# Kernel optimization log

Hardware: AMD Instinct MI355X
Metric: run time of the kernel (lower is better)

## Reference

```python
import jax, jax.numpy as jnp
import numpy as np
import math

FS = 9          # gaussian filter_size
STD = 1.0
LOW = 0.1       # min(threshold1, threshold2)
HIGH = 0.3      # max(threshold1, threshold2)
PAD_G = FS // 2


def _gauss_window(M, std):
    # scipy.signal.windows.gaussian: exp(-0.5*(n/std)^2), n centered, unnormalized
    n = np.arange(M, dtype=np.float64) - (M - 1) / 2.0
    return np.exp(-0.5 * (n / std) ** 2).astype(np.float32)


def _conv(x, w, pad):
    # torch F.conv2d == cross-correlation, NCHW / OIHW
    return jax.lax.conv_general_dilated(
        x, w, window_strides=(1, 1), padding=pad,
        dimension_numbers=("NCHW", "OIHW", "NCHW"))


def setup_inputs() -> dict:
    key = jax.random.key(0)
    img = jax.random.uniform(key, (8, 3, 512, 512), dtype=jnp.float32)
    g = _gauss_window(FS, STD)
    gauss_h = jnp.asarray(g[None, None, None, :])          # [1,1,1,9]
    gauss_v = jnp.asarray(g[None, None, :, None])          # [1,1,9,1]
    sobel_h = jnp.array([[[[1., 0., -1.], [2., 0., -2.], [1., 0., -1.]]]], dtype=jnp.float32)
    sobel_v = jnp.array([[[[1., 2., 1.], [0., 0., 0.], [-1., -2., -1.]]]], dtype=jnp.float32)
    d = np.zeros((8, 1, 3, 3), dtype=np.float32)
    d[:, 0, 1, 1] = 1.0
    # neighbor positions (row, col) for the -1 tap, per directional channel
    neigh = [(1, 2), (2, 2), (2, 1), (2, 0), (1, 0), (0, 0), (0, 1), (0, 2)]
    for k, (r, c) in enumerate(neigh):
        d[k, 0, r, c] = -1.0
    directional = jnp.asarray(d)                            # [8,1,3,3]
    connect = jnp.array([[[[1., 1., 1.], [1., 0., 1.], [1., 1., 1.]]]], dtype=jnp.float32)
    return {"img": img, "gauss_h": gauss_h, "gauss_v": gauss_v,
            "sobel_h": sobel_h, "sobel_v": sobel_v,
            "directional": directional, "connect": connect}


def reference(img, gauss_h, gauss_v, sobel_h, sobel_v, directional, connect):
    B, C, H, W = img.shape
    x = img.reshape(B * C, 1, H, W)  # per-channel 1-in/1-out convs, batched
    blur = _conv(_conv(x, gauss_h, [(0, 0), (PAD_G, PAD_G)]),
                 gauss_v, [(PAD_G, PAD_G), (0, 0)])
    gx = _conv(blur, sobel_h, [(1, 1), (1, 1)]).reshape(B, C, H, W)
    gy = _conv(blur, sobel_v, [(1, 1), (1, 1)]).reshape(B, C, H, W)

    # sum of per-channel magnitudes, [B,1,H,W]
    grad_mag = jnp.sqrt(gx * gx + gy * gy).sum(axis=1, keepdims=True)
    ori = jnp.arctan2(gy.sum(axis=1, keepdims=True),
                      gx.sum(axis=1, keepdims=True)) * (180.0 / math.pi) + 180.0
    ori = jnp.round(ori / 45.0) * 45.0

    all_filtered = _conv(grad_mag, directional, [(1, 1), (1, 1)])  # [B,8,H,W]

    pixel_count = B * H * W
    pr = jnp.arange(pixel_count, dtype=jnp.int32)
    flat = all_filtered.reshape(-1)
    # faithful replication of the original's flat linear-index gather
    k_pos = ((ori / 45.0) % 8.0).reshape(-1).astype(jnp.int32)
    k_neg = ((ori / 45.0 + 4.0) % 8.0).reshape(-1).astype(jnp.int32)
    pos = flat[k_pos * pixel_count + pr].reshape(B, 1, H, W)
    neg = flat[k_neg * pixel_count + pr].reshape(B, 1, H, W)

    is_max = jnp.minimum(pos, neg) > 0.0
    thin = jnp.where(is_max, grad_mag, 0.0)

    t = jnp.where(thin < LOW, 0.0, thin)
    higher = thin > HIGH
    t = jnp.where(higher, 1.0, t)
    connect_map = _conv(higher.astype(jnp.float32), connect, [(1, 1), (1, 1)])
    middle = (thin >= LOW) & (thin <= HIGH)
    t = jnp.where(middle, 0.0, t)
    connect_map = jnp.where(middle, connect_map, 0.0)
    t = jnp.where(connect_map > 0.0, 1.0, t)
    # zero borders
    t = t.at[..., 0, :].set(0.0)
    t = t.at[..., -1, :].set(0.0)
    t = t.at[..., :, 0].set(0.0)
    t = t.at[..., :, -1].set(0.0)
    return (t > 0.0).astype(jnp.float32)
```

## Files before the change

kernel.cpp:

```cpp
#include <hip/hip_runtime.h>
#include <math.h>

#define HH 512
#define WW 512
#define NB 8
#define NC 3
#define TILE 32
#define HW (HH*WW)

__global__ __launch_bounds__(256) void canny_gm_kernel(
    const float* __restrict__ img, const float* __restrict__ gwin,
    double* __restrict__ GM, unsigned char* __restrict__ KP)
{
    __shared__ float  simg[42][42];
    __shared__ double shb[42][34];
    __shared__ double sbl[34][34];

    const int tilesX = WW / TILE;
    const int tx0 = (blockIdx.x % tilesX) * TILE;
    const int ty0 = (blockIdx.x / tilesX) * TILE;
    const int b = blockIdx.y;
    const int t = threadIdx.x;

    double g[9];
#pragma unroll
    for (int k = 0; k < 9; ++k) g[k] = (double)gwin[k];

    double mag[4], sgx[4], sgy[4];
#pragma unroll
    for (int p = 0; p < 4; ++p) { mag[p] = 0.0; sgx[p] = 0.0; sgy[p] = 0.0; }

    for (int c = 0; c < NC; ++c) {
        const float* ip = img + ((size_t)b * NC + c) * HW;
        for (int idx = t; idx < 42*42; idx += 256) {
            int r = idx / 42, col = idx % 42;
            int gr = ty0 - 5 + r, gc = tx0 - 5 + col;
            float v = 0.0f;
            if (gr >= 0 && gr < HH && gc >= 0 && gc < WW) v = ip[gr*WW + gc];
            simg[r][col] = v;
        }
        __syncthreads();
        for (int idx = t; idx < 42*34; idx += 256) {
            int r = idx / 34, col = idx % 34;
            double acc = 0.0;
#pragma unroll
            for (int k = 0; k < 9; ++k) acc += g[k] * (double)simg[r][col + k];
            shb[r][col] = acc;
        }
        __syncthreads();
        for (int idx = t; idx < 34*34; idx += 256) {
            int r = idx / 34, col = idx % 34;
            double acc = 0.0;
#pragma unroll
            for (int k = 0; k < 9; ++k) acc += g[k] * shb[r + k][col];
            sbl[r][col] = acc;
        }
        __syncthreads();
#pragma unroll
        for (int p = 0; p < 4; ++p) {
            int pix = t + p * 256;
            int i = pix >> 5, j = pix & 31;
            int gi = ty0 + i, gj = tx0 + j;
            bool up = (gi - 1 >= 0), dn = (gi + 1 < HH), lf = (gj - 1 >= 0), rt = (gj + 1 < WW);
            double tl = (up && lf) ? sbl[i][j]     : 0.0;
            double tc = (up)       ? sbl[i][j+1]   : 0.0;
            double tr = (up && rt) ? sbl[i][j+2]   : 0.0;
            double ml = (lf)       ? sbl[i+1][j]   : 0.0;
            double mr = (rt)       ? sbl[i+1][j+2] : 0.0;
            double bl = (dn && lf) ? sbl[i+2][j]   : 0.0;
            double bc = (dn)       ? sbl[i+2][j+1] : 0.0;
            double br = (dn && rt) ? sbl[i+2][j+2] : 0.0;
            double gx = (tl - tr) + 2.0*(ml - mr) + (bl - br);
            double gy = (tl + 2.0*tc + tr) - (bl + 2.0*bc + br);
            mag[p] += sqrt(gx*gx + gy*gy);
            sgx[p] += gx; sgy[p] += gy;
        }
        __syncthreads();
    }

#pragma unroll
    for (int p = 0; p < 4; ++p) {
        int pix = t + p * 256;
        int i = pix >> 5, j = pix & 31;
        int gi = ty0 + i, gj = tx0 + j;
        size_t o = (size_t)b * HW + (size_t)gi * WW + gj;
        GM[o] = mag[p];
        double ori = atan2(sgy[p], sgx[p]) * (180.0 / M_PI) + 180.0;
        int k = (int)rint(ori / 45.0);
        KP[o] = (unsigned char)(k & 7);
    }
}

__global__ __launch_bounds__(256) void canny_thin_kernel(
    const double* __restrict__ GM, const unsigned char* __restrict__ KP,
    unsigned char* __restrict__ CODE)
{
    int idx = blockIdx.x * blockDim.x + threadIdx.x;
    if (idx >= NB * HW) return;
    int j = idx & (WW - 1);
    int i = (idx >> 9) & (HH - 1);
    int b = idx >> 18;

    const int drt[8] = {0, 1, 1, 1, 0, -1, -1, -1};
    const int dct[8] = {1, 1, 0, -1, -1, -1, 0, 1};

    int kp = KP[idx];
    int kn = (kp + 4) & 7;
    int ni = i + drt[b], nj = j + dct[b];
    bool nin = (ni >= 0 && ni < HH && nj >= 0 && nj < WW);
    size_t p0 = (size_t)i * WW + j;
    size_t pn = (size_t)ni * WW + nj;

    double gmp  = GM[(size_t)kp * HW + p0];
    double gmn  = GM[(size_t)kn * HW + p0];
    double gmpn = nin ? GM[(size_t)kp * HW + pn] : 0.0;
    double gmnn = nin ? GM[(size_t)kn * HW + pn] : 0.0;

    double pos = gmp - gmpn;
    double neg = gmn - gmnn;
    double thin = (fmin(pos, neg) > 0.0) ? GM[idx] : 0.0;

    unsigned char code = 0;
    if (thin > 0.3) code |= 1;
    if (thin >= 0.1 && thin <= 0.3) code |= 2;
    CODE[idx] = code;
}

__global__ __launch_bounds__(256) void canny_out_kernel(
    const unsigned char* __restrict__ CODE, float* __restrict__ out)
{
    int idx = blockIdx.x * blockDim.x + threadIdx.x;
    if (idx >= NB * HW) return;
    int j = idx & (WW - 1);
    int i = (idx >> 9) & (HH - 1);
    int b = idx >> 18;

    float r = 0.0f;
    if (i > 0 && i < HH - 1 && j > 0 && j < WW - 1) {
        unsigned char c = CODE[idx];
        if (c & 1) {
            r = 1.0f;
        } else if (c & 2) {
            const unsigned char* base = CODE + (size_t)b * HW;
            int any = 0;
            any |= base[(size_t)(i-1)*WW + (j-1)] & 1;
            any |= base[(size_t)(i-1)*WW + (j  )] & 1;
            any |= base[(size_t)(i-1)*WW + (j+1)] & 1;
            any |= base[(size_t)(i  )*WW + (j-1)] & 1;
            any |= base[(size_t)(i  )*WW + (j+1)] & 1;
            any |= base[(size_t)(i+1)*WW + (j-1)] & 1;
            any |= base[(size_t)(i+1)*WW + (j  )] & 1;
            any |= base[(size_t)(i+1)*WW + (j+1)] & 1;
            if (any) r = 1.0f;
        }
    }
    out[idx] = r;
}

extern "C" void kernel_launch(void* const* d_in, const int* in_sizes, int n_in,
                              void* d_out, int out_size, void* d_ws, size_t ws_size,
                              hipStream_t stream) {
    const float* img  = (const float*)d_in[0];
    const float* gwin = (const float*)d_in[1];

    double* GM = (double*)d_ws;
    unsigned char* KP = (unsigned char*)d_ws + (size_t)NB * HW * sizeof(double);
    unsigned char* CODE = KP + (size_t)NB * HW;
    float* out = (float*)d_out;

    dim3 g1((HH / TILE) * (WW / TILE), NB);
    canny_gm_kernel<<<g1, 256, 0, stream>>>(img, gwin, GM, KP);

    int nblk = (NB * HW) / 256;
    canny_thin_kernel<<<nblk, 256, 0, stream>>>(GM, KP, CODE);
    canny_out_kernel<<<nblk, 256, 0, stream>>>(CODE, out);
}
```

Measured before the change: 73.58 us.

## Widen blur tile, fuse horizontal pass with global loads, replace atan2 with sector tests

Tiles grow from 32x32 to 64x32. The horizontal Gaussian pass now reads straight from global memory, which drops the float image staging buffer and one sync per channel, and the halo overhead per output pixel shrinks. The atan2-based orientation quantisation becomes comparisons against tan(22.5°) and tan(67.5°). The direction lookup tables in the thin kernel become packed bit constants. Doubles in shared memory grow to about 40KB, which may lower occupancy, and the sector tests must match the rounding of atan2 exactly at boundaries.

```diff
diff --git a/kernel.cpp b/kernel.cpp
--- a/kernel.cpp
+++ b/kernel.cpp
@@ -5,20 +5,27 @@
 #define WW 512
 #define NB 8
 #define NC 3
-#define TILE 32
 #define HW (HH*WW)
+
+#define TX 64
+#define TY 32
+#define HB_ROWS 42
+#define HB_COLS 66
+#define BL_ROWS 34
+#define BL_COLS 66
+#define HB_ITEMS (HB_ROWS*HB_COLS)
+#define BL_ITEMS (BL_ROWS*BL_COLS)
 
 __global__ __launch_bounds__(256) void canny_gm_kernel(
     const float* __restrict__ img, const float* __restrict__ gwin,
     double* __restrict__ GM, unsigned char* __restrict__ KP)
 {
-    __shared__ float  simg[42][42];
-    __shared__ double shb[42][34];
-    __shared__ double sbl[34][34];
-
-    const int tilesX = WW / TILE;
-    const int tx0 = (blockIdx.x % tilesX) * TILE;
-    const int ty0 = (blockIdx.x / tilesX) * TILE;
+    __shared__ double shb[HB_ROWS][HB_COLS];
+    __shared__ double sbl[BL_ROWS][BL_COLS];
+
+    const int tilesX = WW / TX;
+    const int tx0 = (blockIdx.x % tilesX) * TX;
+    const int ty0 = (blockIdx.x / tilesX) * TY;
     const int b = blockIdx.y;
     const int t = threadIdx.x;
 
@@ -26,50 +33,80 @@
 #pragma unroll
     for (int k = 0; k < 9; ++k) g[k] = (double)gwin[k];
 
-    double mag[4], sgx[4], sgy[4];
-#pragma unroll
-    for (int p = 0; p < 4; ++p) { mag[p] = 0.0; sgx[p] = 0.0; sgy[p] = 0.0; }
+    const int jj = t & 63;
+    const int w  = t >> 6;
+
+    double mag[8], sgx[8], sgy[8];
+#pragma unroll
+    for (int p = 0; p < 8; ++p) { mag[p] = 0.0; sgx[p] = 0.0; sgy[p] = 0.0; }
+
+    const bool safeX = (tx0 >= 8) && (tx0 + TX + 8 <= WW);
+
+    const int hr0 = t / HB_COLS, hc0 = t % HB_COLS;
 
     for (int c = 0; c < NC; ++c) {
         const float* ip = img + ((size_t)b * NC + c) * HW;
-        for (int idx = t; idx < 42*42; idx += 256) {
-            int r = idx / 42, col = idx % 42;
-            int gr = ty0 - 5 + r, gc = tx0 - 5 + col;
-            float v = 0.0f;
-            if (gr >= 0 && gr < HH && gc >= 0 && gc < WW) v = ip[gr*WW + gc];
-            simg[r][col] = v;
+
+        {
+            int r = hr0, cc = hc0, idx = t;
+#pragma unroll 1
+            for (int it = 0; it < 11; ++it) {
+                if (idx < HB_ITEMS) {
+                    int gr = ty0 - 5 + r;
+                    double acc = 0.0;
+                    if ((unsigned)gr < (unsigned)HH) {
+                        if (safeX) {
+                            const float* rp = ip + (size_t)gr * WW + (tx0 - 5 + cc);
+#pragma unroll
+                            for (int k = 0; k < 9; ++k) acc += g[k] * (double)rp[k];
+                        } else {
+                            int gcb = tx0 - 5 + cc;
+                            const float* rowp = ip + (size_t)gr * WW;
+#pragma unroll
+                            for (int k = 0; k < 9; ++k) {
+                                int gc = gcb + k;
+                                float v = ((unsigned)gc < (unsigned)WW) ? rowp[gc] : 0.0f;
+                                acc += g[k] * (double)v;
+                            }
+                        }
+                    }
+                    shb[r][cc] = acc;
+                }
+                idx += 256; r += 3; cc += 58;
+                if (cc >= HB_COLS) { cc -= HB_COLS; r += 1; }
+            }
         }
         __syncthreads();
-        for (int idx = t; idx < 42*34; idx += 256) {
-            int r = idx / 34, col = idx % 34;
-            double acc = 0.0;
-#pragma unroll
-            for (int k = 0; k < 9; ++k) acc += g[k] * (double)simg[r][col + k];
-            shb[r][col] = acc;
+
+        {
+            int r = hr0, cc = hc0, idx = t;
+#pragma unroll 1
+            for (int it = 0; it < 9; ++it) {
+                if (idx < BL_ITEMS) {
+                    double acc = 0.0;
+#pragma unroll
+                    for (int k = 0; k < 9; ++k) acc += g[k] * shb[r + k][cc];
+                    sbl[r][cc] = acc;
+                }
+                idx += 256; r += 3; cc += 58;
+                if (cc >= BL_COLS) { cc -= BL_COLS; r += 1; }
+            }
         }
         __syncthreads();
-        for (int idx = t; idx < 34*34; idx += 256) {
-            int r = idx / 34, col = idx % 34;
-            double acc = 0.0;
-#pragma unroll
-            for (int k = 0; k < 9; ++k) acc += g[k] * shb[r + k][col];
-            sbl[r][col] = acc;
-        }
-        __syncthreads();
-#pragma unroll
-        for (int p = 0; p < 4; ++p) {
-            int pix = t + p * 256;
-            int i = pix >> 5, j = pix & 31;
-            int gi = ty0 + i, gj = tx0 + j;
-            bool up = (gi - 1 >= 0), dn = (gi + 1 < HH), lf = (gj - 1 >= 0), rt = (gj + 1 < WW);
-            double tl = (up && lf) ? sbl[i][j]     : 0.0;
-            double tc = (up)       ? sbl[i][j+1]   : 0.0;
-            double tr = (up && rt) ? sbl[i][j+2]   : 0.0;
-            double ml = (lf)       ? sbl[i+1][j]   : 0.0;
-            double mr = (rt)       ? sbl[i+1][j+2] : 0.0;
-            double bl = (dn && lf) ? sbl[i+2][j]   : 0.0;
-            double bc = (dn)       ? sbl[i+2][j+1] : 0.0;
-            double br = (dn && rt) ? sbl[i+2][j+2] : 0.0;
+
+#pragma unroll
+        for (int p = 0; p < 8; ++p) {
+            int i = w + 4 * p;
+            int gi = ty0 + i, gj = tx0 + jj;
+            bool up = (gi >= 1), dn = (gi <= HH - 2), lf = (gj >= 1), rt = (gj <= WW - 2);
+            double tl = (up && lf) ? sbl[i][jj]     : 0.0;
+            double tc = (up)       ? sbl[i][jj+1]   : 0.0;
+            double tr = (up && rt) ? sbl[i][jj+2]   : 0.0;
+            double ml = (lf)       ? sbl[i+1][jj]   : 0.0;
+            double mr = (rt)       ? sbl[i+1][jj+2] : 0.0;
+            double bl = (dn && lf) ? sbl[i+2][jj]   : 0.0;
+            double bc = (dn)       ? sbl[i+2][jj+1] : 0.0;
+            double br = (dn && rt) ? sbl[i+2][jj+2] : 0.0;
             double gx = (tl - tr) + 2.0*(ml - mr) + (bl - br);
             double gy = (tl + 2.0*tc + tr) - (bl + 2.0*bc + br);
             mag[p] += sqrt(gx*gx + gy*gy);
@@ -78,16 +115,21 @@
         __syncthreads();
     }
 
-#pragma unroll
-    for (int p = 0; p < 4; ++p) {
-        int pix = t + p * 256;
-        int i = pix >> 5, j = pix & 31;
-        int gi = ty0 + i, gj = tx0 + j;
-        size_t o = (size_t)b * HW + (size_t)gi * WW + gj;
+    const double t225 = 0.41421356237309503;
+    const double t675 = 2.414213562373095;
+#pragma unroll
+    for (int p = 0; p < 8; ++p) {
+        int i = w + 4 * p;
+        size_t o = (size_t)b * HW + (size_t)(ty0 + i) * WW + (tx0 + jj);
         GM[o] = mag[p];
-        double ori = atan2(sgy[p], sgx[p]) * (180.0 / M_PI) + 180.0;
-        int k = (int)rint(ori / 45.0);
-        KP[o] = (unsigned char)(k & 7);
+        double sx = sgx[p], sy = sgy[p];
+        double ax = fabs(sx), ay = fabs(sy);
+        int kp;
+        if (ay <= ax * t225)      kp = (sx >= 0.0) ? 4 : 0;
+        else if (ay >= ax * t675) kp = (sy > 0.0) ? 6 : 2;
+        else if (sx > 0.0)        kp = (sy > 0.0) ? 5 : 3;
+        else                      kp = (sy > 0.0) ? 7 : 1;
+        KP[o] = (unsigned char)kp;
     }
 }
 
@@ -101,13 +143,13 @@
     int i = (idx >> 9) & (HH - 1);
     int b = idx >> 18;
 
-    const int drt[8] = {0, 1, 1, 1, 0, -1, -1, -1};
-    const int dct[8] = {1, 1, 0, -1, -1, -1, 0, 1};
+    int dr = (int)((0x00012221u >> (b * 4)) & 15u) - 1;
+    int dc = (int)((0x21000122u >> (b * 4)) & 15u) - 1;
 
     int kp = KP[idx];
     int kn = (kp + 4) & 7;
-    int ni = i + drt[b], nj = j + dct[b];
-    bool nin = (ni >= 0 && ni < HH && nj >= 0 && nj < WW);
+    int ni = i + dr, nj = j + dc;
+    bool nin = ((unsigned)ni < (unsigned)HH) && ((unsigned)nj < (unsigned)WW);
     size_t p0 = (size_t)i * WW + j;
     size_t pn = (size_t)ni * WW + nj;
 
@@ -168,7 +210,7 @@
     unsigned char* CODE = KP + (size_t)NB * HW;
     float* out = (float*)d_out;
 
-    dim3 g1((HH / TILE) * (WW / TILE), NB);
+    dim3 g1((WW / TX) * (HH / TY), NB);
     canny_gm_kernel<<<g1, 256, 0, stream>>>(img, gwin, GM, KP);
 
     int nblk = (NB * HW) / 256;
```

Measured after the change: 161.0 us. +118.8%, slower.
